# Kernel tuning notes

Measured on AMD Instinct MI355X. Metric: run time of the kernel, lower is better.

## Reference

```python
import jax, jax.numpy as jnp
import numpy as np
import math

# Config (matches init_kwargs): ProphetNet-style ngram self-attention
T, B, E, H, NGRAM, NB, MAXD = 512, 4, 1024, 16, 2, 32, 128
HD = E // H
TGT = (1 + NGRAM) * T
NEG = -1e9


def _buckets(rel):
    # faithful numpy version of _relative_positions_bucket (bidirectional=False)
    n = np.maximum(-rel, 0)
    max_exact = NB // 2
    is_small = n < max_exact
    large = max_exact + np.log(np.maximum(n, 1) / max_exact) / math.log(MAXD / max_exact) * (NB - max_exact)
    large = np.minimum(large, NB - 1).astype(np.int32)
    return np.where(is_small, n.astype(np.int32), large)


def setup_inputs() -> dict:
    key = jax.random.key(0)
    ks = jax.random.split(key, 4)
    s = 0.02
    # position ids 1..T (ProphetNet positions start at 1); precompute bucket tables
    pos = np.arange(1, T + 1, dtype=np.int64)[None, :].repeat(B, axis=0)          # [B,T]
    main_rel = pos[:, None, :] - pos[:, :, None]                                  # [B,T,T]
    pred_keys = np.concatenate([pos - 1, pos], axis=-1)                           # [B,2T]
    pred_rel = pred_keys[:, None, :] - pos[:, :, None]                            # [B,T,2T]
    return {
        "query": jax.random.normal(ks[0], (TGT, B, E), jnp.float32),
        "in_proj_weight": jax.random.normal(ks[1], (3 * E, E), jnp.float32) * s,
        "in_proj_bias": jnp.zeros((3 * E,), jnp.float32),
        "rel_w": jax.random.normal(ks[2], (NB * H, E), jnp.float32) * s,
        "rel_b": jnp.zeros((NB * H,), jnp.float32),
        "out_w": jax.random.normal(ks[3], (E, E), jnp.float32) * s,
        "out_b": jnp.zeros((E,), jnp.float32),
        "main_buckets": jnp.asarray(_buckets(main_rel), jnp.int32),
        "predict_buckets": jnp.asarray(_buckets(pred_rel), jnp.int32),
    }


def reference(query, in_proj_weight, in_proj_bias, rel_w, rel_b, out_w, out_b,
              main_buckets, predict_buckets):
    scaling = HD ** -0.5
    qkv = query @ in_proj_weight.T + in_proj_bias                  # [TGT,B,3E]
    q, k, v = jnp.split(qkv, 3, axis=-1)
    q = q * scaling

    def heads(x):  # [TGT,B,E] -> [B*H, TGT, HD]
        return x.reshape(TGT, B * H, HD).transpose(1, 0, 2)

    q, k, v = heads(q), heads(k), heads(v)
    q_main, k_main, v_main = q[:, :T], k[:, :T], v[:, :T]

    def ngram_split(x):  # [B*H, NGRAM*T, HD] -> [N, B*H, T, HD]
        return x[:, T:].reshape(B * H, NGRAM, T, HD).transpose(1, 0, 2, 3)

    q_pred, k_pred, v_pred = ngram_split(q), ngram_split(k), ngram_split(v)
    h_main = query[:T]                                             # [T,B,E]
    h_pred = query[T:].reshape(NGRAM, T, B, E)

    # ---------- main stream ----------
    aw_main = jnp.einsum('bth,bsh->bts', q_main, k_main)           # [B*H,T,T]
    vals = h_main.transpose(1, 0, 2) @ rel_w.T + rel_b             # [B,T,NB*H]
    vals = vals.reshape(B, T, NB, H).transpose(0, 3, 1, 2)         # [B,H,T,NB]
    idx = jnp.broadcast_to(main_buckets[:, None], (B, H, T, T))
    rel_main = jnp.take_along_axis(vals, idx, axis=-1).reshape(B * H, T, T)
    causal = jnp.triu(jnp.full((T, T), NEG, jnp.float32), 1)       # self_attn_mask
    aw_main = jax.nn.softmax(aw_main + rel_main + causal[None], axis=-1)
    attn_main = jnp.einsum('bts,bsh->bth', aw_main, v_main)        # [B*H,T,HD]
    attn_main = attn_main.transpose(1, 0, 2).reshape(1, T, B, E)
    attn_main = attn_main @ out_w.T + out_b

    # ---------- ngram predict streams ----------
    k_ng = jnp.concatenate([jnp.broadcast_to(k_main[None], (NGRAM, B * H, T, HD)), k_pred], axis=2)
    v_ng = jnp.concatenate([jnp.broadcast_to(v_main[None], (NGRAM, B * H, T, HD)), v_pred], axis=2)
    aw_ng = jnp.einsum('nbtc,nbsc->nbts', q_pred, k_ng)            # [N,B*H,T,2T]
    valsn = h_pred.transpose(0, 2, 1, 3) @ rel_w.T + rel_b         # [N,B,T,NB*H]
    valsn = valsn.reshape(NGRAM, B, T, NB, H).transpose(0, 1, 4, 2, 3)  # [N,B,H,T,NB]
    idxn = jnp.broadcast_to(predict_buckets[None, :, None], (NGRAM, B, H, T, 2 * T))
    rel_ng = jnp.take_along_axis(valsn, idxn, axis=-1).reshape(NGRAM, B * H, T, 2 * T)
    # ngram_mask: main part causal, predict part only the matching position
    ng_mask = jnp.concatenate([causal, NEG * (1.0 - jnp.eye(T, dtype=jnp.float32))], axis=1)  # [T,2T]
    aw_ng = jax.nn.softmax(aw_ng + rel_ng + ng_mask[None, None], axis=-1)
    attn_ng = jnp.einsum('nbts,nbsc->nbtc', aw_ng, v_ng)           # [N,B*H,T,HD]
    attn_ng = attn_ng.transpose(0, 2, 1, 3).reshape(NGRAM, T, B, E)
    attn_ng = attn_ng @ out_w.T + out_b

    return jnp.concatenate([attn_main, attn_ng], axis=0).reshape(TGT, B, E)
```

## Files before the change

kernel.cpp:

```cpp
#include <hip/hip_runtime.h>
#include <hip/hip_bf16.h>
#include <math.h>

constexpr int T_ = 512;
constexpr int B_ = 4;
constexpr int E_ = 1024;
constexpr int H_ = 16;
constexpr int NGRAM_ = 2;
constexpr int TGT_ = (1 + NGRAM_) * T_;
constexpr int ROWS_ = TGT_ * B_;

typedef __bf16 bf16_t;
typedef __bf16 bf16x8 __attribute__((ext_vector_type(8)));
typedef __bf16 bf16x4 __attribute__((ext_vector_type(4)));
typedef float f32x4 __attribute__((ext_vector_type(4)));

#define GLL(gaddr, laddr)                                                     \
  __builtin_amdgcn_global_load_lds(                                           \
      (const __attribute__((address_space(1))) void*)(gaddr),                 \
      (__attribute__((address_space(3))) void*)(laddr), 16, 0, 0)

#define BARX()   asm volatile("s_barrier" ::: "memory")
#define WVM7()   asm volatile("s_waitcnt vmcnt(7)" ::: "memory")
#define WVM10()  asm volatile("s_waitcnt vmcnt(10)" ::: "memory")
#define WVM0()   asm volatile("s_waitcnt vmcnt(0)" ::: "memory")

__global__ __launch_bounds__(256) void prep(
    const float* __restrict__ query, const float* __restrict__ ipw,
    const float* __restrict__ relw, const float* __restrict__ outw,
    bf16_t* __restrict__ qb, bf16_t* __restrict__ ipwb,
    bf16_t* __restrict__ relwb, bf16_t* __restrict__ outwb) {
  const int i = blockIdx.x * 256 + threadIdx.x;
  constexpr int N1 = ROWS_ * E_ / 4;
  constexpr int N2 = 3 * E_ * E_ / 4;
  constexpr int N3 = 512 * E_ / 4;
  constexpr int N4 = E_ * E_ / 4;
  const float4* src;
  bf16_t* dst;
  int j = i;
  if (i < N1) { src = (const float4*)query; dst = qb; }
  else if (i < N1 + N2) { src = (const float4*)ipw; dst = ipwb; j = i - N1; }
  else if (i < N1 + N2 + N3) { src = (const float4*)relw; dst = relwb; j = i - N1 - N2; }
  else if (i < N1 + N2 + N3 + N4) { src = (const float4*)outw; dst = outwb; j = i - N1 - N2 - N3; }
  else return;
  const float4 v = src[j];
  bf16x4 o;
  o[0] = (bf16_t)v.x; o[1] = (bf16_t)v.y;
  o[2] = (bf16_t)v.z; o[3] = (bf16_t)v.w;
  ((bf16x4*)dst)[j] = o;
}

__device__ __forceinline__ int sw256(int row, int col) {
  return row * 256 + ((((col >> 3) ^ (row & 31)) << 3) | (col & 7));
}

__global__ __launch_bounds__(512, 2) void bgemm_proj(
    const bf16_t* __restrict__ A, const bf16_t* __restrict__ W,
    const float* __restrict__ ipb, const float* __restrict__ relb,
    bf16_t* __restrict__ qkvb, float* __restrict__ relv2,
    bf16_t* __restrict__ vT, int bn0) {
  __shared__ bf16_t smem[57344];
  bf16_t* As0 = smem;
  bf16_t* As1 = smem + 12288;
  bf16_t* Bs0 = smem + 24576;
  bf16_t* Bs1 = smem + 24576 + 16384;

  const int tid = threadIdx.x;
  const int wave = tid >> 6, lane = tid & 63;
  const int wr = wave >> 2, wc = wave & 3;
  const int nx = gridDim.x;
  const int pid = blockIdx.y * nx + blockIdx.x;
  const int chunk = (nx * gridDim.y) >> 3;
  const int lid = (pid & 7) * chunk + (pid >> 3);
  const int by = lid / nx;
  const int bx = lid - by * nx;
  const int bm = by * 192, bn = bn0 + bx * 256;
  const int q = lane >> 4, ln = lane & 15;
  const int grow = tid >> 3;
  const int gcol = ((tid & 7) ^ (grow & 7)) * 8;
  const int co[2] = {((q) ^ (ln & 7)) * 8, ((4 + q) ^ (ln & 7)) * 8};

  f32x4 acc[6][4];
#pragma unroll
  for (int mi = 0; mi < 6; ++mi)
#pragma unroll
    for (int ni = 0; ni < 4; ++ni)
#pragma unroll
      for (int r = 0; r < 4; ++r) acc[mi][ni][r] = 0.f;

  auto stage = [&](int kt, bf16_t* la, bf16_t* lb) {
    const int kc = kt * 64 + gcol;
#pragma unroll
    for (int p = 0; p < 3; ++p)
      GLL(&A[(size_t)(bm + p * 64 + grow) * 1024 + kc], &la[p * 4096 + tid * 8]);
#pragma unroll
    for (int p = 0; p < 4; ++p)
      GLL(&W[(size_t)(bn + p * 64 + grow) * 1024 + kc], &lb[p * 4096 + tid * 8]);
  };

  auto compute_tile = [&](const bf16_t* la, const bf16_t* lb) {
    bf16x8 a0[3], a1[3], b0[4], b1[4];
#pragma unroll
    for (int ni = 0; ni < 4; ++ni)
      b0[ni] = *(const bf16x8*)&lb[(wc * 64 + ni * 16 + ln) * 64 + co[0]];
#pragma unroll
    for (int mi = 0; mi < 3; ++mi)
      a0[mi] = *(const bf16x8*)&la[(wr * 96 + mi * 16 + ln) * 64 + co[0]];
#pragma unroll
    for (int mi = 0; mi < 3; ++mi)
      a1[mi] = *(const bf16x8*)&la[(wr * 96 + (3 + mi) * 16 + ln) * 64 + co[0]];
    __builtin_amdgcn_s_setprio(1);
#pragma unroll
    for (int mi = 0; mi < 3; ++mi)
#pragma unroll
      for (int ni = 0; ni < 4; ++ni)
        acc[mi][ni] = __builtin_amdgcn_mfma_f32_16x16x32_bf16(
            a0[mi], b0[ni], acc[mi][ni], 0, 0, 0);
    __builtin_amdgcn_s_setprio(0);
#pragma unroll
    for (int ni = 0; ni < 4; ++ni)
      b1[ni] = *(const bf16x8*)&lb[(wc * 64 + ni * 16 + ln) * 64 + co[1]];
#pragma unroll
    for (int mi = 0; mi < 3; ++mi)
      a0[mi] = *(const bf16x8*)&la[(wr * 96 + mi * 16 + ln) * 64 + co[1]];
    __builtin_amdgcn_s_setprio(1);
#pragma unroll
    for (int mi = 0; mi < 3; ++mi)
#pragma unroll
      for (int ni = 0; ni < 4; ++ni)
        acc[3 + mi][ni] = __builtin_amdgcn_mfma_f32_16x16x32_bf16(
            a1[mi], b0[ni], acc[3 + mi][ni], 0, 0, 0);
    __builtin_amdgcn_s_setprio(0);
#pragma unroll
    for (int mi = 0; mi < 3; ++mi)
      a1[mi] = *(const bf16x8*)&la[(wr * 96 + (3 + mi) * 16 + ln) * 64 + co[1]];
    __builtin_amdgcn_s_setprio(1);
#pragma unroll
    for (int mi = 0; mi < 3; ++mi)
#pragma unroll
      for (int ni = 0; ni < 4; ++ni)
        acc[mi][ni] = __builtin_amdgcn_mfma_f32_16x16x32_bf16(
            a0[mi], b1[ni], acc[mi][ni], 0, 0, 0);
    __builtin_amdgcn_s_setprio(0);
    __builtin_amdgcn_s_setprio(1);
#pragma unroll
    for (int mi = 0; mi < 3; ++mi)
#pragma unroll
      for (int ni = 0; ni < 4; ++ni)
        acc[3 + mi][ni] = __builtin_amdgcn_mfma_f32_16x16x32_bf16(
            a1[mi], b1[ni], acc[3 + mi][ni], 0, 0, 0);
    __builtin_amdgcn_s_setprio(0);
  };

  stage(0, As0, Bs0);
  stage(1, As1, Bs1);

  for (int kt = 0; kt < 16; kt += 2) {
    WVM7(); BARX();
    compute_tile(As0, Bs0);
    BARX();
    if (kt + 2 < 16) stage(kt + 2, As0, Bs0);
    if (kt < 14) { WVM7(); } else { WVM0(); }
    BARX();
    compute_tile(As1, Bs1);
    BARX();
    if (kt + 3 < 16) stage(kt + 3, As1, Bs1);
  }

  if (bn < 2048) {
    const float sc = (bn < 1024) ? 0.125f : 1.0f;
#pragma unroll
    for (int mi = 0; mi < 6; ++mi) {
#pragma unroll
      for (int ni = 0; ni < 4; ++ni) {
        const int col = bn + wc * 64 + ni * 16 + ln;
        const float bv = ipb[col];
#pragma unroll
        for (int r = 0; r < 4; ++r) {
          const int row = bm + wr * 96 + mi * 16 + q * 4 + r;
          qkvb[(size_t)row * 3072 + col] = (bf16_t)((acc[mi][ni][r] + bv) * sc);
        }
      }
    }
  } else if (bn < 3072) {
    __syncthreads();
#pragma unroll
    for (int mi = 0; mi < 6; ++mi) {
#pragma unroll
      for (int ni = 0; ni < 4; ++ni) {
        const int col_l = wc * 64 + ni * 16 + ln;
        const float bv = ipb[bn + col_l];
#pragma unroll
        for (int r = 0; r < 4; ++r) {
          const int row_l = wr * 96 + mi * 16 + q * 4 + r;
          smem[sw256(row_l, col_l)] = (bf16_t)(acc[mi][ni][r] + bv);
        }
      }
    }
    __syncthreads();
    const int h0 = (bn - 2048) >> 6;
    const int tb0 = bm >> 2;
#pragma unroll
    for (int e = 0; e < 2; ++e) {
      const int task = e * 512 + tid;
      const int b = task & 3;
      const int c = task >> 2;
      const int h = h0 + (c >> 6);
      const int d = c & 63;
      const size_t base = ((size_t)((b * 16 + h) * 64 + d)) * (size_t)TGT_ + tb0;
#pragma unroll
      for (int k = 0; k < 6; ++k) {
        bf16x8 v8;
#pragma unroll
        for (int i = 0; i < 8; ++i)
          v8[i] = smem[sw256((k * 8 + i) * 4 + b, c)];
        *(bf16x8*)&vT[base + k * 8] = v8;
      }
    }
  } else {
    const int cb = bn - 3072 + wc * 64;
    float4 rb4;
#pragma unroll
    for (int ni = 0; ni < 4; ++ni)
      ((float*)&rb4)[ni] = relb[cb + ni * 16 + ln];
    const int bkbase = cb >> 4;
#pragma unroll
    for (int mi = 0; mi < 6; ++mi) {
#pragma unroll
      for (int r = 0; r < 4; ++r) {
        const int row = bm + wr * 96 + mi * 16 + q * 4 + r;
        float4 v;
        v.x = acc[mi][0][r] + rb4.x;
        v.y = acc[mi][1][r] + rb4.y;
        v.z = acc[mi][2][r] + rb4.z;
        v.w = acc[mi][3][r] + rb4.w;
        *(float4*)&relv2[(size_t)row * 512 + ln * 32 + bkbase] = v;
      }
    }
  }
}

__global__ __launch_bounds__(256, 1) void bgemm_out(
    const bf16_t* __restrict__ A, const bf16_t* __restrict__ W,
    const float* __restrict__ bias, float* __restrict__ C) {
  __shared__ bf16_t smem[40960];

  const int tid = threadIdx.x;
  const int wave = tid >> 6, lane = tid & 63;
  const int wr = wave >> 1, wc = wave & 1;
  const int pid = blockIdx.y * 8 + blockIdx.x;
  const int lid = (pid & 7) * 32 + (pid >> 3);
  const int bm = (lid >> 3) * 192, bn = (lid & 7) * 128;
  const int q = lane >> 4, ln = lane & 15;
  const int grow = tid >> 3;
  const int gcol = ((tid & 7) ^ (grow & 7)) * 8;
  const int co[2] = {((q) ^ (ln & 7)) * 8, ((4 + q) ^ (ln & 7)) * 8};

  f32x4 acc[6][4];
#pragma unroll
  for (int mi = 0; mi < 6; ++mi)
#pragma unroll
    for (int ni = 0; ni < 4; ++ni)
#pragma unroll
      for (int r = 0; r < 4; ++r) acc[mi][ni][r] = 0.f;

  auto stage = [&](int kt) {
    bf16_t* s = smem + (kt & 1) * 20480;
    const int kc = kt * 64 + gcol;
#pragma unroll
    for (int p = 0; p < 6; ++p)
      GLL(&A[(size_t)(bm + p * 32 + grow) * 1024 + kc], &s[p * 2048 + tid * 8]);
#pragma unroll
    for (int p = 0; p < 4; ++p)
      GLL(&W[(size_t)(bn + p * 32 + grow) * 1024 + kc],
          &s[12288 + p * 2048 + tid * 8]);
  };

  auto compute_tile = [&](int kt) {
    const bf16_t* la = smem + (kt & 1) * 20480;
    const bf16_t* lb = la + 12288;
    bf16x8 a0[3], a1[3], b0[4], b1[4];
#pragma unroll
    for (int ni = 0; ni < 4; ++ni)
      b0[ni] = *(const bf16x8*)&lb[(wc * 64 + ni * 16 + ln) * 64 + co[0]];
#pragma unroll
    for (int mi = 0; mi < 3; ++mi)
      a0[mi] = *(const bf16x8*)&la[(wr * 96 + mi * 16 + ln) * 64 + co[0]];
#pragma unroll
    for (int mi = 0; mi < 3; ++mi)
      a1[mi] = *(const bf16x8*)&la[(wr * 96 + (3 + mi) * 16 + ln) * 64 + co[0]];
    __builtin_amdgcn_s_setprio(1);
#pragma unroll
    for (int mi = 0; mi < 3; ++mi)
#pragma unroll
      for (int ni = 0; ni < 4; ++ni)
        acc[mi][ni] = __builtin_amdgcn_mfma_f32_16x16x32_bf16(
            a0[mi], b0[ni], acc[mi][ni], 0, 0, 0);
    __builtin_amdgcn_s_setprio(0);
#pragma unroll
    for (int ni = 0; ni < 4; ++ni)
      b1[ni] = *(const bf16x8*)&lb[(wc * 64 + ni * 16 + ln) * 64 + co[1]];
#pragma unroll
    for (int mi = 0; mi < 3; ++mi)
      a0[mi] = *(const bf16x8*)&la[(wr * 96 + mi * 16 + ln) * 64 + co[1]];
    __builtin_amdgcn_s_setprio(1);
#pragma unroll
    for (int mi = 0; mi < 3; ++mi)
#pragma unroll
      for (int ni = 0; ni < 4; ++ni)
        acc[3 + mi][ni] = __builtin_amdgcn_mfma_f32_16x16x32_bf16(
            a1[mi], b0[ni], acc[3 + mi][ni], 0, 0, 0);
    __builtin_amdgcn_s_setprio(0);
#pragma unroll
    for (int mi = 0; mi < 3; ++mi)
      a1[mi] = *(const bf16x8*)&la[(wr * 96 + (3 + mi) * 16 + ln) * 64 + co[1]];
    __builtin_amdgcn_s_setprio(1);
#pragma unroll
    for (int mi = 0; mi < 3; ++mi)
#pragma unroll
      for (int ni = 0; ni < 4; ++ni)
        acc[mi][ni] = __builtin_amdgcn_mfma_f32_16x16x32_bf16(
            a0[mi], b1[ni], acc[mi][ni], 0, 0, 0);
    __builtin_amdgcn_s_setprio(0);
    __builtin_amdgcn_s_setprio(1);
#pragma unroll
    for (int mi = 0; mi < 3; ++mi)
#pragma unroll
      for (int ni = 0; ni < 4; ++ni)
        acc[3 + mi][ni] = __builtin_amdgcn_mfma_f32_16x16x32_bf16(
            a1[mi], b1[ni], acc[3 + mi][ni], 0, 0, 0);
    __builtin_amdgcn_s_setprio(0);
  };

  stage(0);
  stage(1);

  for (int kt = 0; kt < 16; kt += 2) {
    WVM10(); BARX();
    compute_tile(kt);
    BARX();
    if (kt + 2 < 16) stage(kt + 2);
    if (kt < 14) { WVM10(); } else { WVM0(); }
    BARX();
    compute_tile(kt + 1);
    BARX();
    if (kt + 3 < 16) stage(kt + 3);
  }

#pragma unroll
  for (int mi = 0; mi < 6; ++mi) {
#pragma unroll
    for (int ni = 0; ni < 4; ++ni) {
      const int col = bn + wc * 64 + ni * 16 + ln;
      const float bv = bias[col];
#pragma unroll
      for (int r = 0; r < 4; ++r) {
        const int row = bm + wr * 96 + mi * 16 + q * 4 + r;
        C[(size_t)row * 1024 + col] = acc[mi][ni][r] + bv;
      }
    }
  }
}

__device__ __forceinline__ int bucket_of(int n) {
  if (n < 16) return n;
  const float lf = __log2f((float)n);
  int b = (int)(16.0f + (lf - 4.0f) * 5.3333333f);
  return b > 31 ? 31 : b;
}

__global__ __launch_bounds__(256, 2) void flash_mfma(
    const bf16_t* __restrict__ qkvb, const bf16_t* __restrict__ vT,
    const float* __restrict__ relv2, bf16_t* __restrict__ attn) {
  __shared__ bf16_t Ks[2][64 * 64];
  __shared__ bf16_t Vts[2][64 * 64];
  __shared__ bf16_t Ps[4][16 * 64];
  __shared__ bf16_t biasS[3][64 * 33];

  const int bh = blockIdx.x;
  const int yy = blockIdx.y;
  const int qt = (yy < 4) ? (7 - yy) : (yy - 4);
  const int tq0 = qt * 64;
  const int b = bh >> 4, h = bh & 15;
  const int tid = threadIdx.x;
  const int wave = tid >> 6, lane = tid & 63;
  const int q = lane >> 4, ln = lane & 15;
  const int m0 = wave * 16;
  const int grow = tid >> 3;
  const int gcol = ((tid & 7) ^ (grow & 7)) * 8;
  const int co[2] = {((q) ^ (ln & 7)) * 8, ((4 + q) ^ (ln & 7)) * 8};

#pragma unroll
  for (int z = 0; z < 3; ++z) {
#pragma unroll
    for (int u = 0; u < 2; ++u) {
      const int c = u * 256 + tid;
      const int row = c >> 3, j4 = (c & 7) * 4;
      const float4 v = *(const float4*)
          &relv2[((size_t)(z * T_ + tq0 + row) * B_ + b) * 512 + h * 32 + j4];
      biasS[z][row * 33 + j4 + 0] = (bf16_t)v.x;
      biasS[z][row * 33 + j4 + 1] = (bf16_t)v.y;
      biasS[z][row * 33 + j4 + 2] = (bf16_t)v.z;
      biasS[z][row * 33 + j4 + 3] = (bf16_t)v.w;
    }
  }

#pragma unroll
  for (int u = 0; u < 2; ++u) {
    const int sr = u * 32 + grow;
    GLL(&qkvb[((size_t)(0 * T_ + tq0 + sr) * B_ + b) * 3072 + h * 64 + gcol],
        &Ks[0][u * 2048 + tid * 8]);
    GLL(&qkvb[((size_t)(1 * T_ + tq0 + sr) * B_ + b) * 3072 + h * 64 + gcol],
        &Vts[0][u * 2048 + tid * 8]);
    GLL(&qkvb[((size_t)(2 * T_ + tq0 + sr) * B_ + b) * 3072 + h * 64 + gcol],
        &Ks[1][u * 2048 + tid * 8]);
  }
  __syncthreads();

  bf16x8 aq[3][2];
  aq[0][0] = *(const bf16x8*)&Ks[0][(m0 + ln) * 64 + co[0]];
  aq[0][1] = *(const bf16x8*)&Ks[0][(m0 + ln) * 64 + co[1]];
  aq[1][0] = *(const bf16x8*)&Vts[0][(m0 + ln) * 64 + co[0]];
  aq[1][1] = *(const bf16x8*)&Vts[0][(m0 + ln) * 64 + co[1]];
  aq[2][0] = *(const bf16x8*)&Ks[1][(m0 + ln) * 64 + co[0]];
  aq[2][1] = *(const bf16x8*)&Ks[1][(m0 + ln) * 64 + co[1]];

  float bv31[3][4], bv0[3][4];
#pragma unroll
  for (int z = 0; z < 3; ++z)
#pragma unroll
    for (int r = 0; r < 4; ++r) {
      const int rloc = m0 + q * 4 + r;
      bv31[z][r] = (float)biasS[z][rloc * 33 + 31];
      bv0[z][r] = (float)biasS[z][rloc * 33];
    }

  f32x4 Od[3][4];
  float lpart[3][4];
#pragma unroll
  for (int z = 0; z < 3; ++z)
#pragma unroll
    for (int r = 0; r < 4; ++r) {
      lpart[z][r] = 0.f;
#pragma unroll
      for (int tc = 0; tc < 4; ++tc) Od[z][tc][r] = 0.f;
    }

  const int ntiles = qt + 3;

  auto stage_tile = [&](int jj, int buf) {
    const int krb = (jj <= qt) ? jj * 64 : ((jj - qt) * T_ + tq0);
#pragma unroll
    for (int u = 0; u < 2; ++u) {
      const int sr = u * 32 + grow;
      GLL(&qkvb[((size_t)(krb + sr) * B_ + b) * 3072 + 1024 + h * 64 + gcol],
          &Ks[buf][u * 2048 + tid * 8]);
      GLL(&vT[((size_t)bh * 64 + sr) * (size_t)TGT_ + krb + gcol],
          &Vts[buf][u * 2048 + tid * 8]);
    }
  };

  __syncthreads();
  stage_tile(0, 0);
  __syncthreads();

  for (int jj = 0; jj < ntiles; ++jj) {
    const int cur = jj & 1;
    if (jj + 1 < ntiles) stage_tile(jj + 1, cur ^ 1);

    const int krb = (jj <= qt) ? jj * 64 : ((jj - qt) * T_ + tq0);

    bf16x8 kf[4][2], vf[4][2];
#pragma unroll
    for (int tc = 0; tc < 4; ++tc) {
      kf[tc][0] = *(const bf16x8*)&Ks[cur][(tc * 16 + ln) * 64 + co[0]];
      kf[tc][1] = *(const bf16x8*)&Ks[cur][(tc * 16 + ln) * 64 + co[1]];
      vf[tc][0] = *(const bf16x8*)&Vts[cur][(tc * 16 + ln) * 64 + co[0]];
      vf[tc][1] = *(const bf16x8*)&Vts[cur][(tc * 16 + ln) * 64 + co[1]];
    }

    if (jj <= qt) {
      const bool far = (jj <= qt - 3);
      f32x4 sc[3][4];
#pragma unroll
      for (int z = 0; z < 3; ++z)
#pragma unroll
        for (int tc = 0; tc < 4; ++tc)
#pragma unroll
          for (int r = 0; r < 4; ++r) sc[z][tc][r] = 0.f;
#pragma unroll
      for (int z = 0; z < 3; ++z)
#pragma unroll
        for (int tc = 0; tc < 4; ++tc) {
          sc[z][tc] = __builtin_amdgcn_mfma_f32_16x16x32_bf16(
              aq[z][0], kf[tc][0], sc[z][tc], 0, 0, 0);
          sc[z][tc] = __builtin_amdgcn_mfma_f32_16x16x32_bf16(
              aq[z][1], kf[tc][1], sc[z][tc], 0, 0, 0);
        }

#pragma unroll
      for (int z = 0; z < 3; ++z) {
        if (far) {
#pragma unroll
          for (int r = 0; r < 4; ++r) {
            const float bv = bv31[z][r];
#pragma unroll
            for (int tc = 0; tc < 4; ++tc) {
              const float p = __expf(sc[z][tc][r] + bv);
              lpart[z][r] += p;
              const int pc = (tc * 2 + (ln >> 3)) ^ ((q * 4 + r) & 7);
              Ps[wave][(q * 4 + r) * 64 + pc * 8 + (ln & 7)] = (bf16_t)p;
            }
          }
        } else {
#pragma unroll
          for (int r = 0; r < 4; ++r) {
            const int rloc = m0 + q * 4 + r;
            const int dbase = tq0 + rloc - krb;
#pragma unroll
            for (int tc = 0; tc < 4; ++tc) {
              const int sl = tc * 16 + ln;
              const int d = dbase - sl;
              const bool valid = (jj < qt) | (d >= 0);
              int n = d < 0 ? 0 : d;
              if (z > 0) n += 1;
              const float bv = (float)biasS[z][rloc * 33 + bucket_of(n)];
              const float p = valid ? __expf(sc[z][tc][r] + bv) : 0.f;
              lpart[z][r] += p;
              const int pc = (tc * 2 + (ln >> 3)) ^ ((q * 4 + r) & 7);
              Ps[wave][(q * 4 + r) * 64 + pc * 8 + (ln & 7)] = (bf16_t)p;
            }
          }
        }

        bf16x8 ap[2];
        ap[0] = *(const bf16x8*)&Ps[wave][ln * 64 + co[0]];
        ap[1] = *(const bf16x8*)&Ps[wave][ln * 64 + co[1]];
#pragma unroll
        for (int tc = 0; tc < 4; ++tc) {
          Od[z][tc] = __builtin_amdgcn_mfma_f32_16x16x32_bf16(ap[0], vf[tc][0], Od[z][tc], 0, 0, 0);
          Od[z][tc] = __builtin_amdgcn_mfma_f32_16x16x32_bf16(ap[1], vf[tc][1], Od[z][tc], 0, 0, 0);
        }
      }
    } else {
#pragma unroll
      for (int z = 1; z <= 2; ++z) {
        if (jj - qt == z) {
          f32x4 acc[4];
#pragma unroll
          for (int tc = 0; tc < 4; ++tc)
#pragma unroll
            for (int r = 0; r < 4; ++r) acc[tc][r] = 0.f;
#pragma unroll
          for (int tc = 0; tc < 4; ++tc) {
            acc[tc] = __builtin_amdgcn_mfma_f32_16x16x32_bf16(aq[z][0], kf[tc][0], acc[tc], 0, 0, 0);
            acc[tc] = __builtin_amdgcn_mfma_f32_16x16x32_bf16(aq[z][1], kf[tc][1], acc[tc], 0, 0, 0);
          }
#pragma unroll
          for (int r = 0; r < 4; ++r) {
            const int rloc = m0 + q * 4 + r;
            const float bv = bv0[z][r];
#pragma unroll
            for (int tc = 0; tc < 4; ++tc) {
              const int sl = tc * 16 + ln;
              const float p = (sl == rloc) ? __expf(acc[tc][r] + bv) : 0.f;
              lpart[z][r] += p;
              const int pc = (tc * 2 + (ln >> 3)) ^ ((q * 4 + r) & 7);
              Ps[wave][(q * 4 + r) * 64 + pc * 8 + (ln & 7)] = (bf16_t)p;
            }
          }
          bf16x8 ap[2];
          ap[0] = *(const bf16x8*)&Ps[wave][ln * 64 + co[0]];
          ap[1] = *(const bf16x8*)&Ps[wave][ln * 64 + co[1]];
#pragma unroll
          for (int tc = 0; tc < 4; ++tc) {
            Od[z][tc] = __builtin_amdgcn_mfma_f32_16x16x32_bf16(ap[0], vf[tc][0], Od[z][tc], 0, 0, 0);
            Od[z][tc] = __builtin_amdgcn_mfma_f32_16x16x32_bf16(ap[1], vf[tc][1], Od[z][tc], 0, 0, 0);
          }
        }
      }
    }
    __syncthreads();
  }

#pragma unroll
  for (int z = 0; z < 3; ++z) {
#pragma unroll
    for (int r = 0; r < 4; ++r) {
      float l = lpart[z][r];
      l += __shfl_xor(l, 1, 16);
      l += __shfl_xor(l, 2, 16);
      l += __shfl_xor(l, 4, 16);
      l += __shfl_xor(l, 8, 16);
      const float inv = 1.f / l;
      const size_t rowbase =
          ((size_t)(z * T_ + tq0 + m0 + q * 4 + r) * B_ + b) * (size_t)E_ + h * 64;
#pragma unroll
      for (int tc = 0; tc < 4; ++tc)
        attn[rowbase + tc * 16 + ln] = (bf16_t)(Od[z][tc][r] * inv);
    }
  }
}

extern "C" void kernel_launch(void* const* d_in, const int* in_sizes, int n_in,
                              void* d_out, int out_size, void* d_ws, size_t ws_size,
                              hipStream_t stream) {
  const float* query = (const float*)d_in[0];
  const float* ipw   = (const float*)d_in[1];
  const float* ipb   = (const float*)d_in[2];
  const float* relw  = (const float*)d_in[3];
  const float* relb  = (const float*)d_in[4];
  const float* outw  = (const float*)d_in[5];
  const float* outb  = (const float*)d_in[6];
  float* out = (float*)d_out;

  bf16_t* qkvb  = (bf16_t*)d_ws;
  float*  relv2 = (float*)(qkvb + (size_t)ROWS_ * 3 * E_);
  bf16_t* qb    = (bf16_t*)(relv2 + (size_t)ROWS_ * 512);
  bf16_t* ipwb  = qb + (size_t)ROWS_ * E_;
  bf16_t* relwb = ipwb + (size_t)(3 * E_) * E_;
  bf16_t* outwb = relwb + (size_t)512 * E_;
  bf16_t* attnb = outwb + (size_t)E_ * E_;
  bf16_t* vT    = attnb + (size_t)ROWS_ * E_;

  const dim3 blk(256);

  {
    const int ntot = (ROWS_ * E_ + 3 * E_ * E_ + 512 * E_ + E_ * E_) / 4;
    prep<<<dim3((ntot + 255) / 256), blk, 0, stream>>>(
        query, ipw, relw, outw, qb, ipwb, relwb, outwb);
  }

  bgemm_proj<<<dim3(8, 32), dim3(512), 0, stream>>>(
      qb, ipwb, ipb, relb, qkvb, relv2, vT, 0);
  bgemm_proj<<<dim3(6, 32), dim3(512), 0, stream>>>(
      qb, ipwb, ipb, relb, qkvb, relv2, vT, 2048);

  flash_mfma<<<dim3(64, 8), blk, 0, stream>>>(
      qkvb, vT, relv2, attnb);

  bgemm_out<<<dim3(8, 32), blk, 0, stream>>>(
      attnb, outwb, outb, out);
}
```

Baseline: 233.5 us.

## Split flash attention into 32-row blocks, single-buffer K/V, fold log2e for exp2

The flash attention kernel now uses 128-thread blocks that each handle 32 query rows instead of 64, doubling the grid to 64x16. K/V staging drops from double buffering to a single buffer, with the load for the next tile issued after the compute barrier. The softmax scale and relative-position bias are premultiplied by log2(e) so the kernel can call the hardware exp2 instead of __expf. Smaller blocks with less shared memory should allow more blocks in flight, but each block now reloads the full K/V tiles for only half the rows, and dropping double buffering exposes load latency.

```diff
diff --git a/kernel.cpp b/kernel.cpp
--- a/kernel.cpp
+++ b/kernel.cpp
@@ -24,6 +24,9 @@
 #define WVM7()   asm volatile("s_waitcnt vmcnt(7)" ::: "memory")
 #define WVM10()  asm volatile("s_waitcnt vmcnt(10)" ::: "memory")
 #define WVM0()   asm volatile("s_waitcnt vmcnt(0)" ::: "memory")
+
+constexpr float LOG2E_ = 1.44269504088896f;
+#define EXP2F(x) __builtin_amdgcn_exp2f(x)
 
 __global__ __launch_bounds__(256) void prep(
     const float* __restrict__ query, const float* __restrict__ ipw,
@@ -168,7 +171,7 @@
   }
 
   if (bn < 2048) {
-    const float sc = (bn < 1024) ? 0.125f : 1.0f;
+    const float sc = (bn < 1024) ? 0.125f * LOG2E_ : 1.0f;
 #pragma unroll
     for (int mi = 0; mi < 6; ++mi) {
 #pragma unroll
@@ -369,18 +372,21 @@
   return b > 31 ? 31 : b;
 }
 
-__global__ __launch_bounds__(256, 2) void flash_mfma(
+__global__ __launch_bounds__(128, 3) void flash_mfma(
     const bf16_t* __restrict__ qkvb, const bf16_t* __restrict__ vT,
     const float* __restrict__ relv2, bf16_t* __restrict__ attn) {
-  __shared__ bf16_t Ks[2][64 * 64];
-  __shared__ bf16_t Vts[2][64 * 64];
-  __shared__ bf16_t Ps[4][16 * 64];
-  __shared__ bf16_t biasS[3][64 * 33];
+  __shared__ bf16_t Ks[64 * 64];
+  __shared__ bf16_t Vts[64 * 64];
+  __shared__ bf16_t Ps[2][16 * 64];
+  __shared__ bf16_t biasS[3][32 * 33];
 
   const int bh = blockIdx.x;
   const int yy = blockIdx.y;
-  const int qt = (yy < 4) ? (7 - yy) : (yy - 4);
+  const int rh = yy & 1;
+  const int qy = yy >> 1;
+  const int qt = (qy < 4) ? (7 - qy) : (qy - 4);
   const int tq0 = qt * 64;
+  const int rg0 = tq0 + rh * 32;
   const int b = bh >> 4, h = bh & 15;
   const int tid = threadIdx.x;
   const int wave = tid >> 6, lane = tid & 63;
@@ -394,36 +400,36 @@
   for (int z = 0; z < 3; ++z) {
 #pragma unroll
     for (int u = 0; u < 2; ++u) {
-      const int c = u * 256 + tid;
+      const int c = u * 128 + tid;
       const int row = c >> 3, j4 = (c & 7) * 4;
       const float4 v = *(const float4*)
-          &relv2[((size_t)(z * T_ + tq0 + row) * B_ + b) * 512 + h * 32 + j4];
-      biasS[z][row * 33 + j4 + 0] = (bf16_t)v.x;
-      biasS[z][row * 33 + j4 + 1] = (bf16_t)v.y;
-      biasS[z][row * 33 + j4 + 2] = (bf16_t)v.z;
-      biasS[z][row * 33 + j4 + 3] = (bf16_t)v.w;
+          &relv2[((size_t)(z * T_ + rg0 + row) * B_ + b) * 512 + h * 32 + j4];
+      biasS[z][row * 33 + j4 + 0] = (bf16_t)(v.x * LOG2E_);
+      biasS[z][row * 33 + j4 + 1] = (bf16_t)(v.y * LOG2E_);
+      biasS[z][row * 33 + j4 + 2] = (bf16_t)(v.z * LOG2E_);
+      biasS[z][row * 33 + j4 + 3] = (bf16_t)(v.w * LOG2E_);
     }
   }
 
 #pragma unroll
   for (int u = 0; u < 2; ++u) {
-    const int sr = u * 32 + grow;
-    GLL(&qkvb[((size_t)(0 * T_ + tq0 + sr) * B_ + b) * 3072 + h * 64 + gcol],
-        &Ks[0][u * 2048 + tid * 8]);
-    GLL(&qkvb[((size_t)(1 * T_ + tq0 + sr) * B_ + b) * 3072 + h * 64 + gcol],
-        &Vts[0][u * 2048 + tid * 8]);
-    GLL(&qkvb[((size_t)(2 * T_ + tq0 + sr) * B_ + b) * 3072 + h * 64 + gcol],
-        &Ks[1][u * 2048 + tid * 8]);
+    const int sr = u * 16 + grow;
+    GLL(&qkvb[((size_t)(0 * T_ + rg0 + sr) * B_ + b) * 3072 + h * 64 + gcol],
+        &Ks[u * 1024 + tid * 8]);
+    GLL(&qkvb[((size_t)(1 * T_ + rg0 + sr) * B_ + b) * 3072 + h * 64 + gcol],
+        &Ks[2048 + u * 1024 + tid * 8]);
+    GLL(&qkvb[((size_t)(2 * T_ + rg0 + sr) * B_ + b) * 3072 + h * 64 + gcol],
+        &Vts[u * 1024 + tid * 8]);
   }
   __syncthreads();
 
   bf16x8 aq[3][2];
-  aq[0][0] = *(const bf16x8*)&Ks[0][(m0 + ln) * 64 + co[0]];
-  aq[0][1] = *(const bf16x8*)&Ks[0][(m0 + ln) * 64 + co[1]];
-  aq[1][0] = *(const bf16x8*)&Vts[0][(m0 + ln) * 64 + co[0]];
-  aq[1][1] = *(const bf16x8*)&Vts[0][(m0 + ln) * 64 + co[1]];
-  aq[2][0] = *(const bf16x8*)&Ks[1][(m0 + ln) * 64 + co[0]];
-  aq[2][1] = *(const bf16x8*)&Ks[1][(m0 + ln) * 64 + co[1]];
+  aq[0][0] = *(const bf16x8*)&Ks[(m0 + ln) * 64 + co[0]];
+  aq[0][1] = *(const bf16x8*)&Ks[(m0 + ln) * 64 + co[1]];
+  aq[1][0] = *(const bf16x8*)&Ks[(32 + m0 + ln) * 64 + co[0]];
+  aq[1][1] = *(const bf16x8*)&Ks[(32 + m0 + ln) * 64 + co[1]];
+  aq[2][0] = *(const bf16x8*)&Vts[(m0 + ln) * 64 + co[0]];
+  aq[2][1] = *(const bf16x8*)&Vts[(m0 + ln) * 64 + co[1]];
 
   float bv31[3][4], bv0[3][4];
 #pragma unroll
@@ -448,35 +454,33 @@
 
   const int ntiles = qt + 3;
 
-  auto stage_tile = [&](int jj, int buf) {
+  auto stage_tile = [&](int jj) {
     const int krb = (jj <= qt) ? jj * 64 : ((jj - qt) * T_ + tq0);
 #pragma unroll
-    for (int u = 0; u < 2; ++u) {
-      const int sr = u * 32 + grow;
+    for (int u = 0; u < 4; ++u) {
+      const int sr = u * 16 + grow;
       GLL(&qkvb[((size_t)(krb + sr) * B_ + b) * 3072 + 1024 + h * 64 + gcol],
-          &Ks[buf][u * 2048 + tid * 8]);
+          &Ks[u * 1024 + tid * 8]);
       GLL(&vT[((size_t)bh * 64 + sr) * (size_t)TGT_ + krb + gcol],
-          &Vts[buf][u * 2048 + tid * 8]);
+          &Vts[u * 1024 + tid * 8]);
     }
   };
 
   __syncthreads();
-  stage_tile(0, 0);
-  __syncthreads();
+  stage_tile(0);
 
   for (int jj = 0; jj < ntiles; ++jj) {
-    const int cur = jj & 1;
-    if (jj + 1 < ntiles) stage_tile(jj + 1, cur ^ 1);
+    __syncthreads();
 
     const int krb = (jj <= qt) ? jj * 64 : ((jj - qt) * T_ + tq0);
 
     bf16x8 kf[4][2], vf[4][2];
 #pragma unroll
     for (int tc = 0; tc < 4; ++tc) {
-      kf[tc][0] = *(const bf16x8*)&Ks[cur][(tc * 16 + ln) * 64 + co[0]];
-      kf[tc][1] = *(const bf16x8*)&Ks[cur][(tc * 16 + ln) * 64 + co[1]];
-      vf[tc][0] = *(const bf16x8*)&Vts[cur][(tc * 16 + ln) * 64 + co[0]];
-      vf[tc][1] = *(const bf16x8*)&Vts[cur][(tc * 16 + ln) * 64 + co[1]];
+      kf[tc][0] = *(const bf16x8*)&Ks[(tc * 16 + ln) * 64 + co[0]];
+      kf[tc][1] = *(const bf16x8*)&Ks[(tc * 16 + ln) * 64 + co[1]];
+      vf[tc][0] = *(const bf16x8*)&Vts[(tc * 16 + ln) * 64 + co[0]];
+      vf[tc][1] = *(const bf16x8*)&Vts[(tc * 16 + ln) * 64 + co[1]];
     }
 
     if (jj <= qt) {
@@ -506,7 +510,7 @@
             const float bv = bv31[z][r];
 #pragma unroll
             for (int tc = 0; tc < 4; ++tc) {
-              const float p = __expf(sc[z][tc][r] + bv);
+              const float p = EXP2F(sc[z][tc][r] + bv);
               lpart[z][r] += p;
               const int pc = (tc * 2 + (ln >> 3)) ^ ((q * 4 + r) & 7);
               Ps[wave][(q * 4 + r) * 64 + pc * 8 + (ln & 7)] = (bf16_t)p;
@@ -516,7 +520,7 @@
 #pragma unroll
           for (int r = 0; r < 4; ++r) {
             const int rloc = m0 + q * 4 + r;
-            const int dbase = tq0 + rloc - krb;
+            const int dbase = rg0 + rloc - krb;
 #pragma unroll
             for (int tc = 0; tc < 4; ++tc) {
               const int sl = tc * 16 + ln;
@@ -525,7 +529,7 @@
               int n = d < 0 ? 0 : d;
               if (z > 0) n += 1;
               const float bv = (float)biasS[z][rloc * 33 + bucket_of(n)];
-              const float p = valid ? __expf(sc[z][tc][r] + bv) : 0.f;
+              const float p = valid ? EXP2F(sc[z][tc][r] + bv) : 0.f;
               lpart[z][r] += p;
               const int pc = (tc * 2 + (ln >> 3)) ^ ((q * 4 + r) & 7);
               Ps[wave][(q * 4 + r) * 64 + pc * 8 + (ln & 7)] = (bf16_t)p;
@@ -559,11 +563,12 @@
 #pragma unroll
           for (int r = 0; r < 4; ++r) {
             const int rloc = m0 + q * 4 + r;
+            const int rtile = rh * 32 + rloc;
             const float bv = bv0[z][r];
 #pragma unroll
             for (int tc = 0; tc < 4; ++tc) {
               const int sl = tc * 16 + ln;
-              const float p = (sl == rloc) ? __expf(acc[tc][r] + bv) : 0.f;
+              const float p = (sl == rtile) ? EXP2F(acc[tc][r] + bv) : 0.f;
               lpart[z][r] += p;
               const int pc = (tc * 2 + (ln >> 3)) ^ ((q * 4 + r) & 7);
               Ps[wave][(q * 4 + r) * 64 + pc * 8 + (ln & 7)] = (bf16_t)p;
@@ -581,6 +586,7 @@
       }
     }
     __syncthreads();
+    if (jj + 1 < ntiles) stage_tile(jj + 1);
   }
 
 #pragma unroll
@@ -594,7 +600,7 @@
       l += __shfl_xor(l, 8, 16);
       const float inv = 1.f / l;
       const size_t rowbase =
-          ((size_t)(z * T_ + tq0 + m0 + q * 4 + r) * B_ + b) * (size_t)E_ + h * 64;
+          ((size_t)(z * T_ + rg0 + m0 + q * 4 + r) * B_ + b) * (size_t)E_ + h * 64;
 #pragma unroll
       for (int tc = 0; tc < 4; ++tc)
         attn[rowbase + tc * 16 + ln] = (bf16_t)(Od[z][tc][r] * inv);
@@ -636,7 +642,7 @@
   bgemm_proj<<<dim3(6, 32), dim3(512), 0, stream>>>(
       qb, ipwb, ipb, relb, qkvb, relv2, vT, 2048);
 
-  flash_mfma<<<dim3(64, 8), blk, 0, stream>>>(
+  flash_mfma<<<dim3(64, 16), dim3(128), 0, stream>>>(
       qkvb, vT, relv2, attnb);
 
   bgemm_out<<<dim3(8, 32), blk, 0, stream>>>(
```

Measured after the change: 396.2 us. 1.7x slower.
